# Kernel tuning notes

Measured on AMD Instinct MI355X. Metric: run time of the kernel, lower is better.

The kernel has to match this reference:

```python
import jax, jax.numpy as jnp
import numpy as np

B, T, D = 2, 2048, 1024
N_HEADS = 16
HEAD_DIM = D // N_HEADS
HIDDEN = 4 * D
LN_EPS = 1e-6  # flax LayerNorm default


def apply_rotary_pos_emb(x, positions):
    # x: (B, T, H, head_dim); positions: (T,)
    head_dim = x.shape[-1]
    inv_freq = 1.0 / 10000 ** (jnp.arange(0, head_dim, 2).astype(jnp.float32) / head_dim)
    freqs = jnp.outer(positions.astype(jnp.float32), inv_freq)  # (T, head_dim//2)
    cos_emb = jnp.cos(freqs)[None, :, None, :]
    sin_emb = jnp.sin(freqs)[None, :, None, :]
    x1 = x[..., : head_dim // 2]
    x2 = x[..., head_dim // 2 :]
    return jnp.concatenate([x1 * cos_emb - x2 * sin_emb,
                            x1 * sin_emb + x2 * cos_emb], axis=-1)


def layernorm(x, scale, bias):
    mu = jnp.mean(x, axis=-1, keepdims=True)
    var = jnp.mean(jnp.square(x - mu), axis=-1, keepdims=True)
    return (x - mu) * jax.lax.rsqrt(var + LN_EPS) * scale + bias


def setup_inputs() -> dict:
    key = jax.random.key(0)
    ks = jax.random.split(key, 8)
    lecun = lambda k, shape: jax.random.normal(k, shape, jnp.float32) * (1.0 / np.sqrt(shape[0]))
    x = jax.random.normal(ks[0], (B, T, D), jnp.float32)
    positions = jnp.arange(T, dtype=jnp.int32)
    mask = jnp.tril(jnp.ones((T, T), dtype=bool))[None, None]  # causal (1,1,T,T)
    return {
        "x": x,
        "positions": positions,
        "mask": mask,
        "ln1_scale": jnp.ones((D,), jnp.float32),
        "ln1_bias": jnp.zeros((D,), jnp.float32),
        "w_qkv": lecun(ks[1], (D, 3 * D)),
        "w_o": lecun(ks[2], (D, D)),
        "ln2_scale": jnp.ones((D,), jnp.float32),
        "ln2_bias": jnp.zeros((D,), jnp.float32),
        "w1": lecun(ks[3], (D, HIDDEN)),
        "b1": jnp.zeros((HIDDEN,), jnp.float32),
        "w2": lecun(ks[4], (HIDDEN, D)),
        "b2": jnp.zeros((D,), jnp.float32),
    }


def reference(x, positions, mask, ln1_scale, ln1_bias, w_qkv, w_o,
              ln2_scale, ln2_bias, w1, b1, w2, b2):
    h = layernorm(x, ln1_scale, ln1_bias)
    qkv = h @ w_qkv  # (B,T,3D)
    qkv = qkv.reshape(B, T, 3, N_HEADS, HEAD_DIM)
    q, k, v = jnp.moveaxis(qkv, 2, 0)  # each (B,T,H,hd)
    q = apply_rotary_pos_emb(q, positions)
    k = apply_rotary_pos_emb(k, positions)
    q = jnp.transpose(q, (0, 2, 1, 3))  # (B,H,T,hd)
    k = jnp.transpose(k, (0, 2, 1, 3))
    v = jnp.transpose(v, (0, 2, 1, 3))
    scale = 1.0 / jnp.sqrt(jnp.float32(HEAD_DIM))
    attn_weights = jnp.einsum('bhqd,bhkd->bhqk', q, k) * scale
    attn_weights = jnp.where(mask, attn_weights, -1e10)
    attn_weights = jax.nn.softmax(attn_weights, axis=-1)
    h = jnp.einsum('bhqk,bhkd->bhqd', attn_weights, v)
    h = jnp.transpose(h, (0, 2, 1, 3)).reshape(B, T, D)
    h = h @ w_o
    x = x + h
    h = layernorm(x, ln2_scale, ln2_bias)
    h = jax.nn.gelu(h @ w1 + b1)  # approximate gelu, matching flax nn.gelu default
    h = h @ w2 + b2
    return x + h
```

## Files before the change

kernel.cpp:

```cpp
#include <hip/hip_runtime.h>


typedef __bf16 bf16_t;
typedef bf16_t bf16x8 __attribute__((ext_vector_type(8)));
typedef float f32x4 __attribute__((ext_vector_type(4)));

#define M_ROWS 4096
#define DMODEL 1024
#define TSEQ   2048
#define NHEAD  16
#define HDIM   64

__device__ __forceinline__ ushort f2bf(float f) {
  union { float f; unsigned u; } v; v.f = f;
  unsigned r = (v.u + 0x7fffu + ((v.u >> 16) & 1u)) >> 16;
  return (ushort)r;
}
__device__ __forceinline__ float bf2f(ushort u) {
  union { unsigned u; float f; } v; v.u = ((unsigned)u) << 16;
  return v.f;
}
__device__ __forceinline__ unsigned cvt_pk_bf16(float a, float b) {
  unsigned r;
  asm("v_cvt_pk_bf16_f32 %0, %1, %2" : "=v"(r) : "v"(a), "v"(b));
  return r;
}
__device__ __forceinline__ void gload_lds16(const void* g, void* l) {
  __builtin_amdgcn_global_load_lds(
      (const __attribute__((address_space(1))) unsigned*)g,
      (__attribute__((address_space(3))) unsigned*)l, 16, 0, 0);
}
__device__ __forceinline__ f32x4 mfma16(bf16x8 a, bf16x8 b, f32x4 c) {
  return __builtin_amdgcn_mfma_f32_16x16x32_bf16(a, b, c, 0, 0, 0);
}
__device__ __forceinline__ float gelu_f(float x) {
  float y = 0.7978845608028654f * (x + 0.044715f * x * x * x);
  float e = __expf(2.0f * y);
  float t = 1.0f - 2.0f / (e + 1.0f);
  return 0.5f * x * (1.0f + t);
}

__global__ __launch_bounds__(256)
void transpose_bf16(const float* __restrict__ src, ushort* __restrict__ dst,
                    int K, int N) {
  __shared__ float t[32][33];
  int n0 = blockIdx.x * 32, k0 = blockIdx.y * 32;
  int tx = threadIdx.x & 31, ty = threadIdx.x >> 5;
#pragma unroll
  for (int i = 0; i < 4; i++) {
    int k = ty + i * 8;
    t[k][tx] = src[(size_t)(k0 + k) * N + n0 + tx];
  }
  __syncthreads();
#pragma unroll
  for (int i = 0; i < 4; i++) {
    int nn = ty + i * 8;
    dst[(size_t)(n0 + nn) * K + k0 + tx] = f2bf(t[tx][nn]);
  }
}

__global__ __launch_bounds__(256)
void ln_kernel(const float* __restrict__ x, const float* __restrict__ sc,
               const float* __restrict__ bi, ushort* __restrict__ out) {
  int row = blockIdx.x;
  int tid = threadIdx.x;
  const float4 v = *(const float4*)&x[(size_t)row * DMODEL + tid * 4];
  float s = v.x + v.y + v.z + v.w;
  float s2 = v.x * v.x + v.y * v.y + v.z * v.z + v.w * v.w;
#pragma unroll
  for (int off = 32; off > 0; off >>= 1) {
    s += __shfl_down(s, off);
    s2 += __shfl_down(s2, off);
  }
  __shared__ float red[8];
  int lane = tid & 63, w = tid >> 6;
  if (lane == 0) { red[w * 2] = s; red[w * 2 + 1] = s2; }
  __syncthreads();
  float S = red[0] + red[2] + red[4] + red[6];
  float S2 = red[1] + red[3] + red[5] + red[7];
  float mu = S * (1.0f / DMODEL);
  float var = S2 * (1.0f / DMODEL) - mu * mu;
  float rs = rsqrtf(var + 1e-6f);
  float4 scv = *(const float4*)&sc[tid * 4];
  float4 biv = *(const float4*)&bi[tid * 4];
  ushort4 o;
  o.x = f2bf((v.x - mu) * rs * scv.x + biv.x);
  o.y = f2bf((v.y - mu) * rs * scv.y + biv.y);
  o.z = f2bf((v.z - mu) * rs * scv.z + biv.z);
  o.w = f2bf((v.w - mu) * rs * scv.w + biv.w);
  *(ushort4*)&out[(size_t)row * DMODEL + tid * 4] = o;
}

__global__ __launch_bounds__(256)
void rope_table(const int* __restrict__ positions, float2* __restrict__ tab) {
  int i = blockIdx.x * 256 + threadIdx.x;
  int t = i >> 5, f = i & 31;
  float inv = __expf(-(float)f * (1.0f / 32.0f) * 9.210340371976184f);
  float a = (float)positions[t] * inv;
  tab[i] = make_float2(cosf(a), sinf(a));
}

__global__ __launch_bounds__(256)
void rope_apply(const ushort* __restrict__ qkv, const float2* __restrict__ tab,
                ushort* __restrict__ Q, ushort* __restrict__ Kd,
                ushort* __restrict__ VT) {
  __shared__ ushort vt[64][66];
  int t0 = blockIdx.x * 64;
  int bh = blockIdx.y;
  int b = bh >> 4, h = bh & 15;
  int f = threadIdx.x & 31, tg = threadIdx.x >> 5;
#pragma unroll
  for (int i = 0; i < 8; i++) {
    int tt = tg * 8 + i;
    int t = t0 + tt;
    const ushort* qr = qkv + (size_t)(b * TSEQ + t) * 3072 + h * 64 + f;
    float2 cs = tab[t * 32 + f];
    float c = cs.x, s = cs.y;
    float q1 = bf2f(qr[0]),    q2 = bf2f(qr[32]);
    float k1 = bf2f(qr[1024]), k2 = bf2f(qr[1056]);
    ushort* Qp = Q + ((size_t)bh * TSEQ + t) * HDIM;
    ushort* Kp = Kd + ((size_t)bh * TSEQ + t) * HDIM;
    Qp[f]      = f2bf(q1 * c - q2 * s);
    Qp[f + 32] = f2bf(q1 * s + q2 * c);
    Kp[f]      = f2bf(k1 * c - k2 * s);
    Kp[f + 32] = f2bf(k1 * s + k2 * c);
    vt[f][tt]      = qr[2048];
    vt[f + 32][tt] = qr[2080];
  }
  __syncthreads();
  int t = threadIdx.x & 63, fg = threadIdx.x >> 6;
  ushort* Vp = VT + (size_t)bh * HDIM * TSEQ + t0 + t;
#pragma unroll
  for (int j = 0; j < 16; j++) {
    int ff = fg * 16 + j;
    Vp[(size_t)ff * TSEQ] = vt[ff][t];
  }
}

__global__ __launch_bounds__(256, 4)
void attn_kernel(const ushort* __restrict__ Q, const ushort* __restrict__ Kd,
                 const ushort* __restrict__ VT, ushort* __restrict__ O) {
  int bh = blockIdx.x;
  int qb = 31 - (int)blockIdx.y;
  int nt = qb + 1;
  int tid = threadIdx.x;
  int lane = tid & 63, w = tid >> 6;
  int qw = qb * 64 + w * 16;
  int lr = lane & 15, lg = lane >> 4;
  int q_abs = qw + lr;

  const ushort* Qb = Q + (size_t)bh * TSEQ * HDIM;
  const ushort* Kb = Kd + (size_t)bh * TSEQ * HDIM;
  const ushort* Vb = VT + (size_t)bh * HDIM * TSEQ;

  __shared__ ushort lK[2][64 * 64];
  __shared__ ushort lV[2][64 * 64];
  __shared__ ushort pt[4][16 * 64];
  ushort* myp = pt[w];

  int srow0 = tid >> 3, sch = tid & 7;

  auto stage = [&](int buf, int kt) {
#pragma unroll
    for (int c = 0; c < 2; c++) {
      int r = c * 32 + srow0;
      int gch = sch ^ (r & 7);
      gload_lds16(Kb + (size_t)(kt + r) * HDIM + gch * 8,
                  &lK[buf][c * 2048 + tid * 8]);
      gload_lds16(Vb + (size_t)r * TSEQ + kt + gch * 8,
                  &lV[buf][c * 2048 + tid * 8]);
    }
  };

  const float QS = 0.125f * 1.44269504088896340736f;
  bf16x8 aq0 = *(const bf16x8*)&Qb[(size_t)q_abs * HDIM + lg * 8];
  bf16x8 aq1 = *(const bf16x8*)&Qb[(size_t)q_abs * HDIM + 32 + lg * 8];
#pragma unroll
  for (int j = 0; j < 8; j++) {
    aq0[j] = (bf16_t)((float)aq0[j] * QS);
    aq1[j] = (bf16_t)((float)aq1[j] * QS);
  }

  float m_run = -1e30f, l_run = 0.0f;
  f32x4 o[4] = {};

  stage(0, 0);
  __syncthreads();

  for (int it = 0; it < nt; ++it) {
    int kt = it * 64;
    int buf = it & 1;
    bool diag = (it == nt - 1);

    if (it + 1 < nt) stage(buf ^ 1, kt + 64);

    f32x4 sa[4];
#pragma unroll
    for (int cb = 0; cb < 4; cb++) {
      int row = cb * 16 + lr;
      const ushort* kp = &lK[buf][row * 64];
      bf16x8 k0 = *(const bf16x8*)(kp + (((lg    ) ^ (row & 7)) << 3));
      bf16x8 k1 = *(const bf16x8*)(kp + (((lg + 4) ^ (row & 7)) << 3));
      f32x4 z = {};
      z = mfma16(k0, aq0, z);
      sa[cb] = mfma16(k1, aq1, z);
    }

    if (diag) {
#pragma unroll
      for (int cb = 0; cb < 4; cb++)
#pragma unroll
        for (int r = 0; r < 4; r++)
          if (kt + cb * 16 + lg * 4 + r > q_abs) sa[cb][r] = -1e30f;
    }

    f32x4 m4;
#pragma unroll
    for (int r = 0; r < 4; r++)
      m4[r] = fmaxf(fmaxf(sa[0][r], sa[1][r]), fmaxf(sa[2][r], sa[3][r]));
    float mx = fmaxf(fmaxf(m4[0], m4[1]), fmaxf(m4[2], m4[3]));
    mx = fmaxf(mx, __shfl_xor(mx, 16, 64));
    mx = fmaxf(mx, __shfl_xor(mx, 32, 64));
    float mn = fmaxf(m_run, mx);
    float rescale = __builtin_amdgcn_exp2f(m_run - mn);
    m_run = mn;

    float ps = 0.0f;
    uint2 pk[4];
#pragma unroll
    for (int cb = 0; cb < 4; cb++) {
      float p0 = __builtin_amdgcn_exp2f(sa[cb][0] - mn);
      float p1 = __builtin_amdgcn_exp2f(sa[cb][1] - mn);
      float p2 = __builtin_amdgcn_exp2f(sa[cb][2] - mn);
      float p3 = __builtin_amdgcn_exp2f(sa[cb][3] - mn);
      ps += (p0 + p1) + (p2 + p3);
      pk[cb].x = cvt_pk_bf16(p0, p1);
      pk[cb].y = cvt_pk_bf16(p2, p3);
    }
    ps += __shfl_xor(ps, 16, 64);
    ps += __shfl_xor(ps, 32, 64);
    l_run = l_run * rescale + ps;

#pragma unroll
    for (int cb = 0; cb < 4; cb++)
      *(uint2*)&myp[lr * 64 + (((cb * 4 + lg) ^ lr) << 2)] = pk[cb];

#pragma unroll
    for (int d = 0; d < 4; d++)
#pragma unroll
      for (int r = 0; r < 4; r++) o[d][r] *= rescale;

    union U8 { uint2 h[2]; bf16x8 v; };
    U8 t0, t1;
    t0.h[0] = *(const uint2*)&myp[lr * 64 + (((lg * 2    ) ^ lr) << 2)];
    t0.h[1] = *(const uint2*)&myp[lr * 64 + (((lg * 2 + 1) ^ lr) << 2)];
    t1.h[0] = *(const uint2*)&myp[lr * 64 + (((8 + lg * 2    ) ^ lr) << 2)];
    t1.h[1] = *(const uint2*)&myp[lr * 64 + (((8 + lg * 2 + 1) ^ lr) << 2)];

#pragma unroll
    for (int d = 0; d < 4; d++) {
      int row = d * 16 + lr;
      const ushort* vp = &lV[buf][row * 64];
      bf16x8 va0 = *(const bf16x8*)(vp + (((lg    ) ^ (row & 7)) << 3));
      bf16x8 va1 = *(const bf16x8*)(vp + (((lg + 4) ^ (row & 7)) << 3));
      o[d] = mfma16(va0, t0.v, o[d]);
      o[d] = mfma16(va1, t1.v, o[d]);
    }

    __syncthreads();
  }

  int b = bh >> 4, h = bh & 15;
  float linv = 1.0f / l_run;
  size_t obase = (size_t)(b * TSEQ + qw + lr) * DMODEL + h * 64;
#pragma unroll
  for (int d = 0; d < 4; d++) {
    uint2 st;
    st.x = cvt_pk_bf16(o[d][0] * linv, o[d][1] * linv);
    st.y = cvt_pk_bf16(o[d][2] * linv, o[d][3] * linv);
    *(uint2*)&O[obase + d * 16 + lg * 4] = st;
  }
}

template <int EPI>
__global__ __launch_bounds__(512)
void gemm256(const ushort* __restrict__ A, const ushort* __restrict__ Bt,
             void* __restrict__ Cout, const float* __restrict__ bias,
             const float* __restrict__ resid, int M, int N, int K, int nbn) {
  extern __shared__ ushort smem[];
  ushort* lA = smem;
  ushort* lB = smem + 32768;

  int tid = threadIdx.x;
  int lane = tid & 63, w = tid >> 6;
  int wm = w >> 2, wn = w & 3;
  int lrow = lane & 15, lg = lane >> 4;

  int nwg = gridDim.x;
  int cpx = nwg >> 3;
  int wg = ((int)blockIdx.x & 7) * cpx + ((int)blockIdx.x >> 3);
  int bm = wg / nbn, bn = wg % nbn;

  const ushort* Ab = A + (size_t)bm * 256 * K;
  const ushort* Bb = Bt + (size_t)bn * 256 * K;
  int srow = tid >> 3, sch = tid & 7;

  auto stage = [&](int buf, int k0) {
#pragma unroll
    for (int c = 0; c < 4; c++) {
      int r = c * 64 + srow;
      int gch = sch ^ (r & 7);
      gload_lds16(Ab + (size_t)r * K + k0 + gch * 8,
                  &lA[buf * 16384 + c * 4096 + tid * 8]);
    }
#pragma unroll
    for (int c = 0; c < 4; c++) {
      int r = c * 64 + srow;
      int gch = sch ^ (r & 7);
      gload_lds16(Bb + (size_t)r * K + k0 + gch * 8,
                  &lB[buf * 16384 + c * 4096 + tid * 8]);
    }
  };

  f32x4 acc[8][4] = {};

  int nt = K >> 6;
  stage(0, 0);
  __syncthreads();

  for (int t = 0; t < nt; ++t) {
    int cur = t & 1;
    const ushort* la = &lA[cur * 16384];
    const ushort* lb = &lB[cur * 16384];

    bf16x8 af[8], bf[4];
#pragma unroll
    for (int m = 0; m < 8; m++) {
      int row = wm * 128 + m * 16 + lrow;
      af[m] = *(const bf16x8*)&la[row * 64 + ((lg ^ (row & 7)) << 3)];
    }
#pragma unroll
    for (int n = 0; n < 4; n++) {
      int row = wn * 64 + n * 16 + lrow;
      bf[n] = *(const bf16x8*)&lb[row * 64 + ((lg ^ (row & 7)) << 3)];
    }

    if (t + 1 < nt) stage(cur ^ 1, (t + 1) << 6);

    __builtin_amdgcn_s_setprio(1);
#pragma unroll
    for (int m = 0; m < 8; m++)
#pragma unroll
      for (int n = 0; n < 4; n++)
        acc[m][n] = mfma16(af[m], bf[n], acc[m][n]);
    __builtin_amdgcn_s_setprio(0);

#pragma unroll
    for (int m = 0; m < 8; m++) {
      int row = wm * 128 + m * 16 + lrow;
      af[m] = *(const bf16x8*)&la[row * 64 + (((4 + lg) ^ (row & 7)) << 3)];
    }
#pragma unroll
    for (int n = 0; n < 4; n++) {
      int row = wn * 64 + n * 16 + lrow;
      bf[n] = *(const bf16x8*)&lb[row * 64 + (((4 + lg) ^ (row & 7)) << 3)];
    }
    __builtin_amdgcn_s_setprio(1);
#pragma unroll
    for (int m = 0; m < 8; m++)
#pragma unroll
      for (int n = 0; n < 4; n++)
        acc[m][n] = mfma16(af[m], bf[n], acc[m][n]);
    __builtin_amdgcn_s_setprio(0);

    __builtin_amdgcn_sched_barrier(0);
    asm volatile("s_waitcnt vmcnt(0)" ::: "memory");
    __builtin_amdgcn_s_barrier();
  }

#pragma unroll
  for (int m = 0; m < 8; m++) {
    int rbase = bm * 256 + wm * 128 + m * 16 + lg * 4;
#pragma unroll
    for (int n = 0; n < 4; n++) {
      int c = bn * 256 + wn * 64 + n * 16 + lrow;
#pragma unroll
      for (int r = 0; r < 4; r++) {
        float v = acc[m][n][r];
        size_t idx = (size_t)(rbase + r) * N + c;
        if constexpr (EPI == 0) {
          ((ushort*)Cout)[idx] = f2bf(v);
        } else if constexpr (EPI == 1) {
          ((float*)Cout)[idx] = v + resid[idx];
        } else if constexpr (EPI == 2) {
          ((ushort*)Cout)[idx] = f2bf(gelu_f(v + bias[c]));
        } else {
          ((float*)Cout)[idx] = v + bias[c] + resid[idx];
        }
      }
    }
  }
}

template <int EPI, int BN>
__global__ __launch_bounds__(256)
void gemm_kernel(const ushort* __restrict__ A, const ushort* __restrict__ Bt,
                 void* __restrict__ Cout, const float* __restrict__ bias,
                 const float* __restrict__ resid, int M, int N, int K,
                 int nbn) {
  constexpr int NF = BN / 32;
  __shared__ ushort lA[2][128 * 64];
  __shared__ ushort lB[2][BN * 64];
  int tid = threadIdx.x;
  int lane = tid & 63, w = tid >> 6;
  int wm = w >> 1, wn = w & 1;

  int nwg = gridDim.x;
  int cpx = nwg >> 3;
  int wg = ((int)blockIdx.x & 7) * cpx + ((int)blockIdx.x >> 3);
  int bm = wg / nbn, bn = wg % nbn;

  f32x4 acc[4][NF] = {};

  const ushort* Ab = A + (size_t)bm * 128 * K;
  const ushort* Bb = Bt + (size_t)bn * BN * K;
  int lrow = lane & 15, lg = lane >> 4;
  int srow = tid >> 3, sch = tid & 7;

  auto stage = [&](int buf, int k0) {
#pragma unroll
    for (int c = 0; c < 4; c++) {
      int r = c * 32 + srow;
      int gch = sch ^ (r & 7);
      gload_lds16(Ab + (size_t)r * K + k0 + gch * 8,
                  &lA[buf][c * 2048 + tid * 8]);
    }
#pragma unroll
    for (int c = 0; c < NF; c++) {
      int r = c * 32 + srow;
      int gch = sch ^ (r & 7);
      gload_lds16(Bb + (size_t)r * K + k0 + gch * 8,
                  &lB[buf][c * 2048 + tid * 8]);
    }
  };

  int nt = K >> 6;
  stage(0, 0);
  __syncthreads();

  for (int t = 0; t < nt; ++t) {
    int cur = t & 1;

    bf16x8 af0[4], af1[4], bf0[NF], bf1[NF];
#pragma unroll
    for (int m = 0; m < 4; m++) {
      int row = wm * 64 + m * 16 + lrow;
      const ushort* p = &lA[cur][row * 64];
      af0[m] = *(const bf16x8*)(p + (((lg    ) ^ (row & 7)) << 3));
      af1[m] = *(const bf16x8*)(p + (((lg + 4) ^ (row & 7)) << 3));
    }
#pragma unroll
    for (int n = 0; n < NF; n++) {
      int row = wn * (BN / 2) + n * 16 + lrow;
      const ushort* p = &lB[cur][row * 64];
      bf0[n] = *(const bf16x8*)(p + (((lg    ) ^ (row & 7)) << 3));
      bf1[n] = *(const bf16x8*)(p + (((lg + 4) ^ (row & 7)) << 3));
    }

    if (t + 1 < nt) stage(cur ^ 1, (t + 1) << 6);

    __builtin_amdgcn_s_setprio(1);
#pragma unroll
    for (int m = 0; m < 4; m++)
#pragma unroll
      for (int n = 0; n < NF; n++)
        acc[m][n] = mfma16(af0[m], bf0[n], acc[m][n]);
#pragma unroll
    for (int m = 0; m < 4; m++)
#pragma unroll
      for (int n = 0; n < NF; n++)
        acc[m][n] = mfma16(af1[m], bf1[n], acc[m][n]);
    __builtin_amdgcn_s_setprio(0);

    __builtin_amdgcn_sched_barrier(0);
    asm volatile("s_waitcnt vmcnt(0)" ::: "memory");
    __builtin_amdgcn_s_barrier();
  }

#pragma unroll
  for (int m = 0; m < 4; m++) {
    int rbase = bm * 128 + wm * 64 + m * 16 + (lane >> 4) * 4;
#pragma unroll
    for (int n = 0; n < NF; n++) {
      int c = bn * BN + wn * (BN / 2) + n * 16 + (lane & 15);
#pragma unroll
      for (int r = 0; r < 4; r++) {
        float v = acc[m][n][r];
        size_t idx = (size_t)(rbase + r) * N + c;
        if constexpr (EPI == 0) {
          ((ushort*)Cout)[idx] = f2bf(v);
        } else if constexpr (EPI == 1) {
          ((float*)Cout)[idx] = v + resid[idx];
        } else if constexpr (EPI == 2) {
          ((ushort*)Cout)[idx] = f2bf(gelu_f(v + bias[c]));
        } else {
          ((float*)Cout)[idx] = v + bias[c] + resid[idx];
        }
      }
    }
  }
}

extern "C" void kernel_launch(void* const* d_in, const int* in_sizes, int n_in,
                              void* d_out, int out_size, void* d_ws,
                              size_t ws_size, hipStream_t stream) {
  const float* x      = (const float*)d_in[0];
  const int* positions = (const int*)d_in[1];
  const float* ln1_s  = (const float*)d_in[3];
  const float* ln1_b  = (const float*)d_in[4];
  const float* w_qkv  = (const float*)d_in[5];
  const float* w_o    = (const float*)d_in[6];
  const float* ln2_s  = (const float*)d_in[7];
  const float* ln2_b  = (const float*)d_in[8];
  const float* w1     = (const float*)d_in[9];
  const float* b1     = (const float*)d_in[10];
  const float* w2     = (const float*)d_in[11];
  const float* b2     = (const float*)d_in[12];
  float* out = (float*)d_out;

  char* ws = (char*)d_ws;
  size_t off = 0;
  auto nxt = [&](size_t bytes) {
    char* p = ws + off;
    off += (bytes + 255) & ~(size_t)255;
    return p;
  };
  ushort* wqkvT = (ushort*)nxt(3072ULL * 1024 * 2);
  ushort* woT   = (ushort*)nxt(1024ULL * 1024 * 2);
  ushort* w1T   = (ushort*)nxt(4096ULL * 1024 * 2);
  ushort* w2T   = (ushort*)nxt(1024ULL * 4096 * 2);
  ushort* h1    = (ushort*)nxt((size_t)M_ROWS * DMODEL * 2);
  ushort* qkv   = (ushort*)nxt((size_t)M_ROWS * 3072 * 2);
  ushort* Qb    = (ushort*)nxt(2ULL * NHEAD * TSEQ * HDIM * 2);
  ushort* Kb    = (ushort*)nxt(2ULL * NHEAD * TSEQ * HDIM * 2);
  ushort* VTb   = (ushort*)nxt(2ULL * NHEAD * TSEQ * HDIM * 2);
  ushort* attn  = (ushort*)nxt((size_t)M_ROWS * DMODEL * 2);
  float*  x2    = (float*)nxt((size_t)M_ROWS * DMODEL * 4);
  ushort* h2    = (ushort*)nxt((size_t)M_ROWS * DMODEL * 2);
  ushort* mid   = (ushort*)nxt((size_t)M_ROWS * 4096 * 2);
  float2* tab   = (float2*)nxt((size_t)TSEQ * 32 * 8);

  (void)hipFuncSetAttribute((const void*)gemm256<0>,
                            hipFuncAttributeMaxDynamicSharedMemorySize, 131072);
  (void)hipFuncSetAttribute((const void*)gemm256<2>,
                            hipFuncAttributeMaxDynamicSharedMemorySize, 131072);

  transpose_bf16<<<dim3(3072 / 32, 1024 / 32), 256, 0, stream>>>(w_qkv, wqkvT, 1024, 3072);
  transpose_bf16<<<dim3(1024 / 32, 1024 / 32), 256, 0, stream>>>(w_o, woT, 1024, 1024);
  transpose_bf16<<<dim3(4096 / 32, 1024 / 32), 256, 0, stream>>>(w1, w1T, 1024, 4096);
  transpose_bf16<<<dim3(1024 / 32, 4096 / 32), 256, 0, stream>>>(w2, w2T, 4096, 1024);
  rope_table<<<(TSEQ * 32) / 256, 256, 0, stream>>>(positions, tab);
  ln_kernel<<<M_ROWS, 256, 0, stream>>>(x, ln1_s, ln1_b, h1);
  gemm256<0><<<192, 512, 131072, stream>>>(h1, wqkvT, qkv, nullptr, nullptr, 4096, 3072, 1024, 12);
  rope_apply<<<dim3(TSEQ / 64, 2 * NHEAD), 256, 0, stream>>>(qkv, tab, Qb, Kb, VTb);
  attn_kernel<<<dim3(32, 32), 256, 0, stream>>>(Qb, Kb, VTb, attn);
  gemm_kernel<1, 64><<<512, 256, 0, stream>>>(attn, woT, x2, nullptr, x, 4096, 1024, 1024, 16);
  ln_kernel<<<M_ROWS, 256, 0, stream>>>(x2, ln2_s, ln2_b, h2);
  gemm256<2><<<256, 512, 131072, stream>>>(h2, w1T, mid, b1, nullptr, 4096, 4096, 1024, 16);
  gemm_kernel<3, 64><<<512, 256, 0, stream>>>(mid, w2T, out, b2, x2, 4096, 1024, 4096, 16);
}
```

Measured before the change: 224.2 us.

## Split GEMM fragment loads into halves with barrier ping-pong for two blocks/CU

The 256x256 GEMM kernel now requests two workgroups per CU via launch bounds. To fit the register budget it loads A fragments in two halves of four instead of eight. It also interleaves workgroup barriers between the LDS-load and MFMA phases, in the style of the ping-pong schedule where one block computes while the other loads. This trades extra barriers and more LDS read phases for higher occupancy and overlap. Register pressure from the 128 accumulators may still cause spills.

```diff
diff --git a/kernel.cpp b/kernel.cpp
--- a/kernel.cpp
+++ b/kernel.cpp
@@ -283,7 +283,7 @@
 }
 
 template <int EPI>
-__global__ __launch_bounds__(512)
+__global__ __launch_bounds__(512, 2)
 void gemm256(const ushort* __restrict__ A, const ushort* __restrict__ Bt,
              void* __restrict__ Cout, const float* __restrict__ bias,
              const float* __restrict__ resid, int M, int N, int K, int nbn) {
@@ -323,54 +323,86 @@
   };
 
   f32x4 acc[8][4] = {};
-
   int nt = K >> 6;
+
   stage(0, 0);
+  asm volatile("s_waitcnt vmcnt(0)" ::: "memory");
   __syncthreads();
 
   for (int t = 0; t < nt; ++t) {
     int cur = t & 1;
     const ushort* la = &lA[cur * 16384];
     const ushort* lb = &lB[cur * 16384];
-
-    bf16x8 af[8], bf[4];
-#pragma unroll
-    for (int m = 0; m < 8; m++) {
+    bf16x8 af[4], bfr[4];
+
+#pragma unroll
+    for (int m = 0; m < 4; m++) {
       int row = wm * 128 + m * 16 + lrow;
       af[m] = *(const bf16x8*)&la[row * 64 + ((lg ^ (row & 7)) << 3)];
     }
 #pragma unroll
     for (int n = 0; n < 4; n++) {
       int row = wn * 64 + n * 16 + lrow;
-      bf[n] = *(const bf16x8*)&lb[row * 64 + ((lg ^ (row & 7)) << 3)];
-    }
-
+      bfr[n] = *(const bf16x8*)&lb[row * 64 + ((lg ^ (row & 7)) << 3)];
+    }
     if (t + 1 < nt) stage(cur ^ 1, (t + 1) << 6);
-
+    __builtin_amdgcn_s_barrier();
     __builtin_amdgcn_s_setprio(1);
 #pragma unroll
-    for (int m = 0; m < 8; m++)
+    for (int m = 0; m < 4; m++)
 #pragma unroll
       for (int n = 0; n < 4; n++)
-        acc[m][n] = mfma16(af[m], bf[n], acc[m][n]);
+        acc[m][n] = mfma16(af[m], bfr[n], acc[m][n]);
     __builtin_amdgcn_s_setprio(0);
-
-#pragma unroll
-    for (int m = 0; m < 8; m++) {
+    __builtin_amdgcn_s_barrier();
+
+#pragma unroll
+    for (int m = 0; m < 4; m++) {
+      int row = wm * 128 + (m + 4) * 16 + lrow;
+      af[m] = *(const bf16x8*)&la[row * 64 + ((lg ^ (row & 7)) << 3)];
+    }
+    __builtin_amdgcn_s_barrier();
+    __builtin_amdgcn_s_setprio(1);
+#pragma unroll
+    for (int m = 0; m < 4; m++)
+#pragma unroll
+      for (int n = 0; n < 4; n++)
+        acc[m + 4][n] = mfma16(af[m], bfr[n], acc[m + 4][n]);
+    __builtin_amdgcn_s_setprio(0);
+    __builtin_amdgcn_s_barrier();
+
+#pragma unroll
+    for (int m = 0; m < 4; m++) {
       int row = wm * 128 + m * 16 + lrow;
       af[m] = *(const bf16x8*)&la[row * 64 + (((4 + lg) ^ (row & 7)) << 3)];
     }
 #pragma unroll
     for (int n = 0; n < 4; n++) {
       int row = wn * 64 + n * 16 + lrow;
-      bf[n] = *(const bf16x8*)&lb[row * 64 + (((4 + lg) ^ (row & 7)) << 3)];
-    }
+      bfr[n] = *(const bf16x8*)&lb[row * 64 + (((4 + lg) ^ (row & 7)) << 3)];
+    }
+    __builtin_amdgcn_s_barrier();
     __builtin_amdgcn_s_setprio(1);
 #pragma unroll
-    for (int m = 0; m < 8; m++)
+    for (int m = 0; m < 4; m++)
 #pragma unroll
       for (int n = 0; n < 4; n++)
-        acc[m][n] = mfma16(af[m], bf[n], acc[m][n]);
+        acc[m][n] = mfma16(af[m], bfr[n], acc[m][n]);
+    __builtin_amdgcn_s_setprio(0);
+    __builtin_amdgcn_s_barrier();
+
+#pragma unroll
+    for (int m = 0; m < 4; m++) {
+      int row = wm * 128 + (m + 4) * 16 + lrow;
+      af[m] = *(const bf16x8*)&la[row * 64 + (((4 + lg) ^ (row & 7)) << 3)];
+    }
+    __builtin_amdgcn_s_barrier();
+    __builtin_amdgcn_s_setprio(1);
+#pragma unroll
+    for (int m = 0; m < 4; m++)
+#pragma unroll
+      for (int n = 0; n < 4; n++)
+        acc[m + 4][n] = mfma16(af[m], bfr[n], acc[m + 4][n]);
     __builtin_amdgcn_s_setprio(0);
 
     __builtin_amdgcn_sched_barrier(0);
```

After: 227.7 us. No clear change (+1.5%).

## Deepen gemm256 prefetch to two tiles ahead with split staging

Applied to the files above, without the earlier changes.

Restructures the 256x256 GEMM main loop so global-to-LDS loads run two K-tiles ahead instead of one. Prefetch of tile t+2 goes into the buffer just consumed and is split into chunks issued between the two MFMA halves. Waits use a partial vmcnt instead of draining all loads each iteration. This aims to hide global memory latency behind MFMA work, at the cost of extra barriers and more intricate buffer-reuse ordering.

```diff
diff --git a/kernel.cpp b/kernel.cpp
--- a/kernel.cpp
+++ b/kernel.cpp
@@ -284,9 +284,9 @@
 
 template <int EPI>
 __global__ __launch_bounds__(512)
-void gemm256(const ushort* __restrict__ A, const ushort* __restrict__ Bt,
-             void* __restrict__ Cout, const float* __restrict__ bias,
-             const float* __restrict__ resid, int M, int N, int K, int nbn) {
+void gemm256p(const ushort* __restrict__ A, const ushort* __restrict__ Bt,
+              void* __restrict__ Cout, const float* __restrict__ bias,
+              const float* __restrict__ resid, int M, int N, int K, int nbn) {
   extern __shared__ ushort smem[];
   ushort* lA = smem;
   ushort* lB = smem + 32768;
@@ -305,77 +305,95 @@
   const ushort* Bb = Bt + (size_t)bn * 256 * K;
   int srow = tid >> 3, sch = tid & 7;
 
-  auto stage = [&](int buf, int k0) {
-#pragma unroll
-    for (int c = 0; c < 4; c++) {
-      int r = c * 64 + srow;
-      int gch = sch ^ (r & 7);
-      gload_lds16(Ab + (size_t)r * K + k0 + gch * 8,
-                  &lA[buf * 16384 + c * 4096 + tid * 8]);
-    }
-#pragma unroll
-    for (int c = 0; c < 4; c++) {
-      int r = c * 64 + srow;
-      int gch = sch ^ (r & 7);
-      gload_lds16(Bb + (size_t)r * K + k0 + gch * 8,
-                  &lB[buf * 16384 + c * 4096 + tid * 8]);
-    }
+  auto stageA = [&](int buf, int k0, int rb) {
+    int r = rb + srow;
+    int gch = sch ^ (r & 7);
+    gload_lds16(Ab + (size_t)r * K + k0 + gch * 8,
+                &lA[buf * 16384 + rb * 64 + tid * 8]);
   };
+  auto stageB = [&](int buf, int k0, int rb) {
+    int r = rb + srow;
+    int gch = sch ^ (r & 7);
+    gload_lds16(Bb + (size_t)r * K + k0 + gch * 8,
+                &lB[buf * 16384 + rb * 64 + tid * 8]);
+  };
 
   f32x4 acc[8][4] = {};
-
   int nt = K >> 6;
-  stage(0, 0);
-  __syncthreads();
+
+  {
+    stageA(0, 0, 0); stageA(0, 0, 64); stageA(0, 0, 128); stageA(0, 0, 192);
+    stageB(0, 0, 0); stageB(0, 0, 64); stageB(0, 0, 128); stageB(0, 0, 192);
+    stageA(1, 64, 0); stageA(1, 64, 64); stageA(1, 64, 128); stageA(1, 64, 192);
+    stageB(1, 64, 0); stageB(1, 64, 64); stageB(1, 64, 128); stageB(1, 64, 192);
+  }
+  asm volatile("s_waitcnt vmcnt(8)" ::: "memory");
+  __builtin_amdgcn_s_barrier();
 
   for (int t = 0; t < nt; ++t) {
-    int cur = t & 1;
-    const ushort* la = &lA[cur * 16384];
-    const ushort* lb = &lB[cur * 16384];
-
-    bf16x8 af[8], bf[4];
-#pragma unroll
-    for (int m = 0; m < 8; m++) {
+    int b = t & 1;
+    const ushort* la = &lA[b * 16384];
+    const ushort* lb = &lB[b * 16384];
+    bool pf = (t + 2 < nt);
+    int k2 = (t + 2) << 6;
+
+    bf16x8 af[4][2], bfr[4][2];
+
+#pragma unroll
+    for (int m = 0; m < 4; m++) {
       int row = wm * 128 + m * 16 + lrow;
-      af[m] = *(const bf16x8*)&la[row * 64 + ((lg ^ (row & 7)) << 3)];
+      const ushort* p = &la[row * 64];
+      af[m][0] = *(const bf16x8*)(p + (((lg    ) ^ (row & 7)) << 3));
+      af[m][1] = *(const bf16x8*)(p + (((lg + 4) ^ (row & 7)) << 3));
     }
 #pragma unroll
     for (int n = 0; n < 4; n++) {
       int row = wn * 64 + n * 16 + lrow;
-      bf[n] = *(const bf16x8*)&lb[row * 64 + ((lg ^ (row & 7)) << 3)];
-    }
-
-    if (t + 1 < nt) stage(cur ^ 1, (t + 1) << 6);
-
+      const ushort* p = &lb[row * 64];
+      bfr[n][0] = *(const bf16x8*)(p + (((lg    ) ^ (row & 7)) << 3));
+      bfr[n][1] = *(const bf16x8*)(p + (((lg + 4) ^ (row & 7)) << 3));
+    }
     __builtin_amdgcn_s_setprio(1);
 #pragma unroll
-    for (int m = 0; m < 8; m++)
-#pragma unroll
-      for (int n = 0; n < 4; n++)
-        acc[m][n] = mfma16(af[m], bf[n], acc[m][n]);
+    for (int m = 0; m < 4; m++)
+#pragma unroll
+      for (int n = 0; n < 4; n++) {
+        acc[m][n] = mfma16(af[m][0], bfr[n][0], acc[m][n]);
+        acc[m][n] = mfma16(af[m][1], bfr[n][1], acc[m][n]);
+      }
     __builtin_amdgcn_s_setprio(0);
-
-#pragma unroll
-    for (int m = 0; m < 8; m++) {
-      int row = wm * 128 + m * 16 + lrow;
-      af[m] = *(const bf16x8*)&la[row * 64 + (((4 + lg) ^ (row & 7)) << 3)];
-    }
-#pragma unroll
-    for (int n = 0; n < 4; n++) {
-      int row = wn * 64 + n * 16 + lrow;
-      bf[n] = *(const bf16x8*)&lb[row * 64 + (((4 + lg) ^ (row & 7)) << 3)];
+    __builtin_amdgcn_s_barrier();
+    asm volatile("" ::: "memory");
+    if (pf) {
+      stageA(b, k2, 0); stageA(b, k2, 128);
+      stageB(b, k2, 0); stageB(b, k2, 64); stageB(b, k2, 128); stageB(b, k2, 192);
+    }
+
+#pragma unroll
+    for (int m = 0; m < 4; m++) {
+      int row = wm * 128 + 64 + m * 16 + lrow;
+      const ushort* p = &la[row * 64];
+      af[m][0] = *(const bf16x8*)(p + (((lg    ) ^ (row & 7)) << 3));
+      af[m][1] = *(const bf16x8*)(p + (((lg + 4) ^ (row & 7)) << 3));
     }
     __builtin_amdgcn_s_setprio(1);
 #pragma unroll
-    for (int m = 0; m < 8; m++)
-#pragma unroll
-      for (int n = 0; n < 4; n++)
-        acc[m][n] = mfma16(af[m], bf[n], acc[m][n]);
+    for (int m = 0; m < 4; m++)
+#pragma unroll
+      for (int n = 0; n < 4; n++) {
+        acc[m + 4][n] = mfma16(af[m][0], bfr[n][0], acc[m + 4][n]);
+        acc[m + 4][n] = mfma16(af[m][1], bfr[n][1], acc[m + 4][n]);
+      }
     __builtin_amdgcn_s_setprio(0);
-
-    __builtin_amdgcn_sched_barrier(0);
-    asm volatile("s_waitcnt vmcnt(0)" ::: "memory");
     __builtin_amdgcn_s_barrier();
+    asm volatile("" ::: "memory");
+    if (pf) { stageA(b, k2, 64); stageA(b, k2, 192); }
+
+    if (t + 1 < nt) {
+      if (pf) asm volatile("s_waitcnt vmcnt(8)" ::: "memory");
+      else    asm volatile("s_waitcnt vmcnt(0)" ::: "memory");
+      __builtin_amdgcn_s_barrier();
+    }
   }
 
 #pragma unroll
@@ -550,9 +568,9 @@
   ushort* mid   = (ushort*)nxt((size_t)M_ROWS * 4096 * 2);
   float2* tab   = (float2*)nxt((size_t)TSEQ * 32 * 8);
 
-  (void)hipFuncSetAttribute((const void*)gemm256<0>,
+  (void)hipFuncSetAttribute((const void*)gemm256p<0>,
                             hipFuncAttributeMaxDynamicSharedMemorySize, 131072);
-  (void)hipFuncSetAttribute((const void*)gemm256<2>,
+  (void)hipFuncSetAttribute((const void*)gemm256p<2>,
                             hipFuncAttributeMaxDynamicSharedMemorySize, 131072);
 
   transpose_bf16<<<dim3(3072 / 32, 1024 / 32), 256, 0, stream>>>(w_qkv, wqkvT, 1024, 3072);
@@ -561,11 +579,11 @@
   transpose_bf16<<<dim3(1024 / 32, 4096 / 32), 256, 0, stream>>>(w2, w2T, 4096, 1024);
   rope_table<<<(TSEQ * 32) / 256, 256, 0, stream>>>(positions, tab);
   ln_kernel<<<M_ROWS, 256, 0, stream>>>(x, ln1_s, ln1_b, h1);
-  gemm256<0><<<192, 512, 131072, stream>>>(h1, wqkvT, qkv, nullptr, nullptr, 4096, 3072, 1024, 12);
+  gemm256p<0><<<192, 512, 131072, stream>>>(h1, wqkvT, qkv, nullptr, nullptr, 4096, 3072, 1024, 12);
   rope_apply<<<dim3(TSEQ / 64, 2 * NHEAD), 256, 0, stream>>>(qkv, tab, Qb, Kb, VTb);
   attn_kernel<<<dim3(32, 32), 256, 0, stream>>>(Qb, Kb, VTb, attn);
   gemm_kernel<1, 64><<<512, 256, 0, stream>>>(attn, woT, x2, nullptr, x, 4096, 1024, 1024, 16);
   ln_kernel<<<M_ROWS, 256, 0, stream>>>(x2, ln2_s, ln2_b, h2);
-  gemm256<2><<<256, 512, 131072, stream>>>(h2, w1T, mid, b1, nullptr, 4096, 4096, 1024, 16);
+  gemm256p<2><<<256, 512, 131072, stream>>>(h2, w1T, mid, b1, nullptr, 4096, 4096, 1024, 16);
   gemm_kernel<3, 64><<<512, 256, 0, stream>>>(mid, w2T, out, b2, x2, 4096, 1024, 4096, 16);
 }
```

Result: no change. 222.1 us (-0.9%).
